# Kernel tuning notes

Measured on AMD Instinct MI355X. Metric: run time of the kernel, lower is better.

Reference implementation:

```python
import jax, jax.numpy as jnp
import numpy as np

B, S, D_IN = 256, 1024, 64
H, W_H = 256, 512
W_Y, D_OUT = 256, 64


def setup_inputs() -> dict:
    key = jax.random.key(0)
    ks = jax.random.split(key, 5)
    sc = lambda fan_in: 1.0 / np.sqrt(fan_in)
    return {
        "x": jax.random.normal(ks[0], (B, S, D_IN), dtype=jnp.float32),
        "W1h": jax.random.normal(ks[1], (H + D_IN, W_H), dtype=jnp.float32) * sc(H + D_IN),
        "b1h": jnp.zeros((W_H,), jnp.float32),
        "W2h": jax.random.normal(ks[2], (W_H, H), dtype=jnp.float32) * sc(W_H),
        "b2h": jnp.zeros((H,), jnp.float32),
        "W1y": jax.random.normal(ks[3], (H, W_Y), dtype=jnp.float32) * sc(H),
        "b1y": jnp.zeros((W_Y,), jnp.float32),
        "W2y": jax.random.normal(ks[4], (W_Y, D_OUT), dtype=jnp.float32) * sc(W_Y),
        "b2y": jnp.zeros((D_OUT,), jnp.float32),
    }


def reference(x, W1h, b1h, W2h, b2h, W1y, b1y, W2y, b2y):
    # h_t = hmlp([h_{t-1}, x_t]);  y_t = ymlp(h_t)
    batch = x.shape[0]
    h0 = jnp.zeros((batch, H), x.dtype)

    def step(h, x_t):
        hx = jnp.concatenate([h, x_t], axis=1)          # [B, H+D_IN]
        h_new = jax.nn.silu(hx @ W1h + b1h) @ W2h + b2h  # [B, H]
        y = jax.nn.silu(h_new @ W1y + b1y) @ W2y + b2y   # [B, D_OUT]
        return h_new, (y, h_new)

    xs = jnp.swapaxes(x, 0, 1)                          # [S, B, D_IN]
    _, (ys, hs) = jax.lax.scan(step, h0, xs)
    outs = jnp.swapaxes(ys, 0, 1)                        # [B, S, D_OUT]
    hiddens = jnp.concatenate([h0[None], hs], axis=0)    # [S+1, B, H]
    return outs, hiddens
```

## Files before the change

### kernel.cpp

```cpp
#include <hip/hip_runtime.h>


typedef __bf16 bf16;
typedef __bf16 bf16x8 __attribute__((ext_vector_type(8)));
typedef float  f32x4  __attribute__((ext_vector_type(4)));

#define MFMA16(a, b, c) __builtin_amdgcn_mfma_f32_16x16x32_bf16((a), (b), (c), 0, 0, 0)

static constexpr int Bz = 256, Sq = 1024, DIN = 64, H = 256, WH = 512, WY = 256, DOUT = 64;
static constexpr int OUTS_N = Bz * Sq * DOUT;
static constexpr int HID_T  = Bz * H;

static constexpr int W1H_OFF = 0;
static constexpr int W1H_CNT = (H + DIN) * WH;
static constexpr int W2H_OFF = W1H_OFF + W1H_CNT;
static constexpr int W2H_CNT = WH * H;
static constexpr int W1Y_OFF = W2H_OFF + W2H_CNT;
static constexpr int W1Y_CNT = H * WY;
static constexpr int W2Y_OFF = W1Y_OFF + W1Y_CNT;
static constexpr int W2Y_CNT = WY * DOUT;
static constexpr int PACK_TOTAL = W2Y_OFF + W2Y_CNT;

static constexpr int HX_LD = 328;
static constexpr int A1_LD = 520;
static constexpr int HB_LD = 264;

__device__ __forceinline__ float silu_f(float z) {
    return z / (1.0f + __expf(-z));
}

__global__ void prep_pack(const float* __restrict__ W1h, const float* __restrict__ W2h,
                          const float* __restrict__ W1y, const float* __restrict__ W2y,
                          bf16* __restrict__ ws) {
    int idx = blockIdx.x * 256 + threadIdx.x;
    if (idx >= PACK_TOTAL) return;
    int r = idx;
    const float* src; int row, col, ld;
    if (idx < W2H_OFF) {
        int j = r & 7; r >>= 3; int L = r & 63; r >>= 6;
        int kc = r % 10, nt = r / 10;
        row = kc * 32 + ((L >> 4) << 3) + j; col = nt * 16 + (L & 15);
        src = W1h; ld = WH;
    } else if (idx < W1Y_OFF) {
        r -= W2H_OFF;
        int j = r & 7; r >>= 3; int L = r & 63; r >>= 6;
        int kc = r & 15, nt = r >> 4;
        row = kc * 32 + ((L >> 4) << 3) + j; col = nt * 16 + (L & 15);
        src = W2h; ld = H;
    } else if (idx < W2Y_OFF) {
        r -= W1Y_OFF;
        int j = r & 7; r >>= 3; int L = r & 63; r >>= 6;
        int kc = r & 7, nt = r >> 3;
        row = kc * 32 + ((L >> 4) << 3) + j; col = nt * 16 + (L & 15);
        src = W1y; ld = WY;
    } else {
        r -= W2Y_OFF;
        int j = r & 7; r >>= 3; int L = r & 63; r >>= 6;
        int kc = r & 7, nt = r >> 3;
        row = kc * 32 + ((L >> 4) << 3) + j; col = nt * 16 + (L & 15);
        src = W2y; ld = DOUT;
    }
    ws[idx] = (bf16)src[row * ld + col];
}

__global__ __launch_bounds__(512, 2) void rnn_recur(
        const float* __restrict__ x, const float* __restrict__ b1h,
        const float* __restrict__ b2h, const bf16* __restrict__ ws,
        float* __restrict__ out) {
    __shared__ __align__(16) bf16 w2l[16 * 8 * 64 * 8];
    __shared__ __align__(16) bf16 hx_s[16 * HX_LD];
    __shared__ __align__(16) bf16 a1_s[16 * A1_LD];

    const int tid = threadIdx.x;
    const int wv = tid >> 6, ln = tid & 63;
    const int quad = ln >> 4, l16 = ln & 15;
    const int wgb = blockIdx.x;
    float* hid = out + OUTS_N;

    for (int i = tid; i < 16 * 256; i += 512) {
        int m = i >> 8, c = i & 255;
        hx_s[m * HX_LD + c] = (bf16)0.0f;
        hid[(wgb * 16 + m) * H + c] = 0.0f;
    }

    for (int u = tid; u < 16 * 8 * 64; u += 512) {
        int nt = u >> 9, kc8 = (u >> 6) & 7, lu = u & 63;
        *(bf16x8*)(w2l + ((size_t)u << 3)) =
            *(const bf16x8*)(ws + W2H_OFF + (((nt * 16 + 8 + kc8) * 64 + lu) << 3));
    }

    bf16x8 w1r[6][4];
#pragma unroll
    for (int kci = 0; kci < 6; kci++)
#pragma unroll
        for (int i = 0; i < 4; i++)
            w1r[kci][i] = *(const bf16x8*)(ws + W1H_OFF + ((((wv * 4 + i) * 10 + 4 + kci) * 64 + ln) << 3));

    bf16x8 w2f[8][2];
#pragma unroll
    for (int kc = 0; kc < 8; kc++)
#pragma unroll
        for (int i = 0; i < 2; i++)
            w2f[kc][i] = *(const bf16x8*)(ws + W2H_OFF + ((((wv * 2 + i) * 16 + kc) * 64 + ln) << 3));

    float bs1[4], bs2[2];
#pragma unroll
    for (int i = 0; i < 4; i++) bs1[i] = b1h[(wv * 4 + i) * 16 + l16];
#pragma unroll
    for (int i = 0; i < 2; i++) bs2[i] = b2h[(wv * 2 + i) * 16 + l16];

    const int mrow = tid >> 5;
    const int i2 = (tid & 31) * 2;
    const float* xrow = x + (size_t)(wgb * 16 + mrow) * (Sq * DIN) + i2;

#define W1HP(i, kc) ((const bf16x8*)(ws + W1H_OFF + ((((wv * 4 + (i)) * 10 + (kc)) * 64 + ln) << 3)))
    bf16x8 sA[4], sB[4];
#pragma unroll
    for (int i = 0; i < 4; i++) sA[i] = *W1HP(i, 0);
#pragma unroll
    for (int i = 0; i < 4; i++) sB[i] = *W1HP(i, 1);

    const f32x4 z4 = {0.0f, 0.0f, 0.0f, 0.0f};
    float2 xv = *(const float2*)(xrow);

#define LDHX(kc) (*(const bf16x8*)(hx_s + l16 * HX_LD + (kc) * 32 + quad * 8))
#define LDA1(kc) (*(const bf16x8*)(a1_s + l16 * A1_LD + (kc) * 32 + quad * 8))

#pragma unroll 1
    for (int t = 0; t < Sq; t++) {
        hx_s[mrow * HX_LD + 256 + i2]     = (bf16)xv.x;
        hx_s[mrow * HX_LD + 256 + i2 + 1] = (bf16)xv.y;
        __syncthreads();

        xv = *(const float2*)(xrow + ((t + 1) & (Sq - 1)) * DIN);

        f32x4 acc1[4] = {z4, z4, z4, z4};
        bf16x8 a;
        a = LDHX(0);
#pragma unroll
        for (int i = 0; i < 4; i++) acc1[i] = MFMA16(a, sA[i], acc1[i]);
#pragma unroll
        for (int i = 0; i < 4; i++) sA[i] = *W1HP(i, 2);
        a = LDHX(1);
#pragma unroll
        for (int i = 0; i < 4; i++) acc1[i] = MFMA16(a, sB[i], acc1[i]);
#pragma unroll
        for (int i = 0; i < 4; i++) sB[i] = *W1HP(i, 3);
        a = LDHX(4);
#pragma unroll
        for (int i = 0; i < 4; i++) acc1[i] = MFMA16(a, w1r[0][i], acc1[i]);
        a = LDHX(5);
#pragma unroll
        for (int i = 0; i < 4; i++) acc1[i] = MFMA16(a, w1r[1][i], acc1[i]);
        a = LDHX(2);
#pragma unroll
        for (int i = 0; i < 4; i++) acc1[i] = MFMA16(a, sA[i], acc1[i]);
        a = LDHX(3);
#pragma unroll
        for (int i = 0; i < 4; i++) acc1[i] = MFMA16(a, sB[i], acc1[i]);
        a = LDHX(6);
#pragma unroll
        for (int i = 0; i < 4; i++) acc1[i] = MFMA16(a, w1r[2][i], acc1[i]);
        a = LDHX(7);
#pragma unroll
        for (int i = 0; i < 4; i++) acc1[i] = MFMA16(a, w1r[3][i], acc1[i]);
        a = LDHX(8);
#pragma unroll
        for (int i = 0; i < 4; i++) acc1[i] = MFMA16(a, w1r[4][i], acc1[i]);
        a = LDHX(9);
#pragma unroll
        for (int i = 0; i < 4; i++) acc1[i] = MFMA16(a, w1r[5][i], acc1[i]);

#pragma unroll
        for (int i = 0; i < 4; i++)
#pragma unroll
            for (int r = 0; r < 4; r++) {
                float s = silu_f(acc1[i][r] + bs1[i]);
                a1_s[(quad * 4 + r) * A1_LD + (wv * 4 + i) * 16 + l16] = (bf16)s;
            }
        __syncthreads();

#pragma unroll
        for (int i = 0; i < 4; i++) sA[i] = *W1HP(i, 0);
#pragma unroll
        for (int i = 0; i < 4; i++) sB[i] = *W1HP(i, 1);

        f32x4 acc2[2] = {z4, z4};
#pragma unroll
        for (int kc = 0; kc < 8; kc++) {
            a = LDA1(kc);
#pragma unroll
            for (int i = 0; i < 2; i++) acc2[i] = MFMA16(a, w2f[kc][i], acc2[i]);
        }
#pragma unroll
        for (int kc = 8; kc < 16; kc++) {
            a = LDA1(kc);
#pragma unroll
            for (int i = 0; i < 2; i++) {
                bf16x8 b = *(const bf16x8*)(w2l + ((((wv * 2 + i) * 8 + (kc - 8)) * 64 + ln) << 3));
                acc2[i] = MFMA16(a, b, acc2[i]);
            }
        }

        float* hdst = hid + (size_t)(t + 1) * HID_T + (wgb * 16) * H;
#pragma unroll
        for (int i = 0; i < 2; i++)
#pragma unroll
            for (int r = 0; r < 4; r++) {
                float h = acc2[i][r] + bs2[i];
                int m = quad * 4 + r, c = (wv * 2 + i) * 16 + l16;
                hdst[m * H + c] = h;
                hx_s[m * HX_LD + c] = (bf16)h;
            }
    }
#undef W1HP
#undef LDHX
#undef LDA1
}

__global__ __launch_bounds__(256) void rnn_ymlp(
        const float* __restrict__ b1y, const float* __restrict__ b2y,
        const bf16* __restrict__ ws, float* __restrict__ out) {
    __shared__ __align__(16) bf16 hb[64 * HB_LD];

    const int tid = threadIdx.x, wv = tid >> 6, ln = tid & 63;
    const int quad = ln >> 4, l16 = ln & 15;
    const int g = blockIdx.x, b = g >> 4, t0 = (g & 15) * 64;
    const float* hid = out + OUTS_N;

    {
        int r = tid >> 2, c0 = (tid & 3) * 64;
        const float* srcr = hid + (size_t)(t0 + 1 + r) * HID_T + b * H + c0;
        bf16* d0 = hb + r * HB_LD + c0;
#pragma unroll
        for (int jj = 0; jj < 16; jj++) {
            float4 v = *(const float4*)(srcr + jj * 4);
            bf16* d = d0 + jj * 4;
            d[0] = (bf16)v.x; d[1] = (bf16)v.y; d[2] = (bf16)v.z; d[3] = (bf16)v.w;
        }
    }
    __syncthreads();

    const f32x4 z4 = {0.0f, 0.0f, 0.0f, 0.0f};
    f32x4 acc[4][4];
#pragma unroll
    for (int i = 0; i < 4; i++)
#pragma unroll
        for (int mt = 0; mt < 4; mt++) acc[i][mt] = z4;
#pragma unroll
    for (int kc = 0; kc < 8; kc++) {
        bf16x8 a[4];
#pragma unroll
        for (int mt = 0; mt < 4; mt++)
            a[mt] = *(const bf16x8*)(hb + (mt * 16 + l16) * HB_LD + kc * 32 + quad * 8);
#pragma unroll
        for (int i = 0; i < 4; i++) {
            bf16x8 bb = *(const bf16x8*)(ws + W1Y_OFF + ((((wv * 4 + i) * 8 + kc) * 64 + ln) << 3));
#pragma unroll
            for (int mt = 0; mt < 4; mt++) acc[i][mt] = MFMA16(a[mt], bb, acc[i][mt]);
        }
    }
    float bias1[4];
#pragma unroll
    for (int i = 0; i < 4; i++) bias1[i] = b1y[(wv * 4 + i) * 16 + l16];
    __syncthreads();

#pragma unroll
    for (int i = 0; i < 4; i++)
#pragma unroll
        for (int mt = 0; mt < 4; mt++)
#pragma unroll
            for (int r = 0; r < 4; r++) {
                float s = silu_f(acc[i][mt][r] + bias1[i]);
                hb[(mt * 16 + quad * 4 + r) * HB_LD + (wv * 4 + i) * 16 + l16] = (bf16)s;
            }
    __syncthreads();

    f32x4 acy[4] = {z4, z4, z4, z4};
#pragma unroll
    for (int kc = 0; kc < 8; kc++) {
        bf16x8 bb = *(const bf16x8*)(ws + W2Y_OFF + (((wv * 8 + kc) * 64 + ln) << 3));
#pragma unroll
        for (int mt = 0; mt < 4; mt++) {
            bf16x8 a = *(const bf16x8*)(hb + (mt * 16 + l16) * HB_LD + kc * 32 + quad * 8);
            acy[mt] = MFMA16(a, bb, acy[mt]);
        }
    }
    float bias2 = b2y[wv * 16 + l16];
    float* ob = out + (size_t)b * (Sq * DOUT);
#pragma unroll
    for (int mt = 0; mt < 4; mt++)
#pragma unroll
        for (int r = 0; r < 4; r++) {
            int m = mt * 16 + quad * 4 + r;
            ob[(t0 + m) * DOUT + wv * 16 + l16] = acy[mt][r] + bias2;
        }
}

extern "C" void kernel_launch(void* const* d_in, const int* in_sizes, int n_in,
                              void* d_out, int out_size, void* d_ws, size_t ws_size,
                              hipStream_t stream) {
    (void)in_sizes; (void)n_in; (void)out_size; (void)ws_size;
    const float* x   = (const float*)d_in[0];
    const float* W1h = (const float*)d_in[1];
    const float* b1h = (const float*)d_in[2];
    const float* W2h = (const float*)d_in[3];
    const float* b2h = (const float*)d_in[4];
    const float* W1y = (const float*)d_in[5];
    const float* b1y = (const float*)d_in[6];
    const float* W2y = (const float*)d_in[7];
    const float* b2y = (const float*)d_in[8];
    float* out = (float*)d_out;
    bf16* ws = (bf16*)d_ws;

    prep_pack<<<(PACK_TOTAL + 255) / 256, 256, 0, stream>>>(W1h, W2h, W1y, W2y, ws);
    rnn_recur<<<16, 512, 0, stream>>>(x, b1h, b2h, ws, out);
    rnn_ymlp<<<4096, 256, 0, stream>>>(b1y, b2y, ws, out);
}
```

Baseline: 4.449 ms.

## Transpose MFMA operands, XOR-swizzle LDS, vectorize stores, fold biases into accumulators

Swaps the A/B operands of every MFMA so each lane owns four consecutive output columns. That allows packed bf16x4 LDS writes and float4 global stores for hidden states and outputs in place of scalar stores. The padded LDS row strides are replaced by an XOR swizzle to avoid bank conflicts, and bias values now initialize the accumulators. One W1h chunk moves from registers to streamed loads, which frees registers but adds one more global load per step.

```diff
diff --git a/kernel.cpp b/kernel.cpp
--- a/kernel.cpp
+++ b/kernel.cpp
@@ -2,6 +2,8 @@
 
 
 typedef __bf16 bf16;
+typedef __bf16 bf16x2 __attribute__((ext_vector_type(2)));
+typedef __bf16 bf16x4 __attribute__((ext_vector_type(4)));
 typedef __bf16 bf16x8 __attribute__((ext_vector_type(8)));
 typedef float  f32x4  __attribute__((ext_vector_type(4)));
 
@@ -21,12 +23,17 @@
 static constexpr int W2Y_CNT = WY * DOUT;
 static constexpr int PACK_TOTAL = W2Y_OFF + W2Y_CNT;
 
-static constexpr int HX_LD = 328;
-static constexpr int A1_LD = 520;
-static constexpr int HB_LD = 264;
-
-__device__ __forceinline__ float silu_f(float z) {
-    return z / (1.0f + __expf(-z));
+static constexpr int HX_LD = 320;
+static constexpr int A1_LD = 512;
+
+__device__ __forceinline__ float silu_f(float z) { return z / (1.0f + __expf(-z)); }
+__device__ __forceinline__ int swz8(int row) { return ((row ^ (row >> 3)) & 7) << 3; }
+
+__device__ __forceinline__ bf16x4 silu4(f32x4 v) {
+    bf16x4 p;
+    p[0] = (bf16)silu_f(v[0]); p[1] = (bf16)silu_f(v[1]);
+    p[2] = (bf16)silu_f(v[2]); p[3] = (bf16)silu_f(v[3]);
+    return p;
 }
 
 __global__ void prep_pack(const float* __restrict__ W1h, const float* __restrict__ W2h,
@@ -74,12 +81,13 @@
     const int tid = threadIdx.x;
     const int wv = tid >> 6, ln = tid & 63;
     const int quad = ln >> 4, l16 = ln & 15;
+    const int swl = swz8(l16);
     const int wgb = blockIdx.x;
     float* hid = out + OUTS_N;
 
+    for (int i = tid; i < 16 * HX_LD; i += 512) hx_s[i] = (bf16)0.0f;
     for (int i = tid; i < 16 * 256; i += 512) {
         int m = i >> 8, c = i & 255;
-        hx_s[m * HX_LD + c] = (bf16)0.0f;
         hid[(wgb * 16 + m) * H + c] = 0.0f;
     }
 
@@ -89,12 +97,12 @@
             *(const bf16x8*)(ws + W2H_OFF + (((nt * 16 + 8 + kc8) * 64 + lu) << 3));
     }
 
-    bf16x8 w1r[6][4];
-#pragma unroll
-    for (int kci = 0; kci < 6; kci++)
+    bf16x8 w1r[5][4];
+#pragma unroll
+    for (int kci = 0; kci < 5; kci++)
 #pragma unroll
         for (int i = 0; i < 4; i++)
-            w1r[kci][i] = *(const bf16x8*)(ws + W1H_OFF + ((((wv * 4 + i) * 10 + 4 + kci) * 64 + ln) << 3));
+            w1r[kci][i] = *(const bf16x8*)(ws + W1H_OFF + ((((wv * 4 + i) * 10 + 5 + kci) * 64 + ln) << 3));
 
     bf16x8 w2f[8][2];
 #pragma unroll
@@ -103,15 +111,22 @@
         for (int i = 0; i < 2; i++)
             w2f[kc][i] = *(const bf16x8*)(ws + W2H_OFF + ((((wv * 2 + i) * 16 + kc) * 64 + ln) << 3));
 
-    float bs1[4], bs2[2];
-#pragma unroll
-    for (int i = 0; i < 4; i++) bs1[i] = b1h[(wv * 4 + i) * 16 + l16];
-#pragma unroll
-    for (int i = 0; i < 2; i++) bs2[i] = b2h[(wv * 2 + i) * 16 + l16];
+    f32x4 bs1[4], bs2[2];
+#pragma unroll
+    for (int i = 0; i < 4; i++) {
+        float4 v = *(const float4*)(b1h + (wv * 4 + i) * 16 + quad * 4);
+        bs1[i][0] = v.x; bs1[i][1] = v.y; bs1[i][2] = v.z; bs1[i][3] = v.w;
+    }
+#pragma unroll
+    for (int i = 0; i < 2; i++) {
+        float4 v = *(const float4*)(b2h + (wv * 2 + i) * 16 + quad * 4);
+        bs2[i][0] = v.x; bs2[i][1] = v.y; bs2[i][2] = v.z; bs2[i][3] = v.w;
+    }
 
     const int mrow = tid >> 5;
     const int i2 = (tid & 31) * 2;
     const float* xrow = x + (size_t)(wgb * 16 + mrow) * (Sq * DIN) + i2;
+    const int xoff = mrow * HX_LD + ((256 + i2) ^ swz8(mrow));
 
 #define W1HP(i, kc) ((const bf16x8*)(ws + W1H_OFF + ((((wv * 4 + (i)) * 10 + (kc)) * 64 + ln) << 3)))
     bf16x8 sA[4], sB[4];
@@ -120,64 +135,61 @@
 #pragma unroll
     for (int i = 0; i < 4; i++) sB[i] = *W1HP(i, 1);
 
-    const f32x4 z4 = {0.0f, 0.0f, 0.0f, 0.0f};
     float2 xv = *(const float2*)(xrow);
 
-#define LDHX(kc) (*(const bf16x8*)(hx_s + l16 * HX_LD + (kc) * 32 + quad * 8))
-#define LDA1(kc) (*(const bf16x8*)(a1_s + l16 * A1_LD + (kc) * 32 + quad * 8))
+#define LDHX(kc) (*(const bf16x8*)(hx_s + l16 * HX_LD + (((kc) * 32 + quad * 8) ^ swl)))
+#define LDA1(kc) (*(const bf16x8*)(a1_s + l16 * A1_LD + (((kc) * 32 + quad * 8) ^ swl)))
 
 #pragma unroll 1
     for (int t = 0; t < Sq; t++) {
-        hx_s[mrow * HX_LD + 256 + i2]     = (bf16)xv.x;
-        hx_s[mrow * HX_LD + 256 + i2 + 1] = (bf16)xv.y;
+        bf16x2 xp; xp[0] = (bf16)xv.x; xp[1] = (bf16)xv.y;
+        *(bf16x2*)(hx_s + xoff) = xp;
         __syncthreads();
 
         xv = *(const float2*)(xrow + ((t + 1) & (Sq - 1)) * DIN);
 
-        f32x4 acc1[4] = {z4, z4, z4, z4};
+        f32x4 acc1[4] = {bs1[0], bs1[1], bs1[2], bs1[3]};
         bf16x8 a;
         a = LDHX(0);
 #pragma unroll
-        for (int i = 0; i < 4; i++) acc1[i] = MFMA16(a, sA[i], acc1[i]);
+        for (int i = 0; i < 4; i++) acc1[i] = MFMA16(sA[i], a, acc1[i]);
 #pragma unroll
         for (int i = 0; i < 4; i++) sA[i] = *W1HP(i, 2);
         a = LDHX(1);
 #pragma unroll
-        for (int i = 0; i < 4; i++) acc1[i] = MFMA16(a, sB[i], acc1[i]);
+        for (int i = 0; i < 4; i++) acc1[i] = MFMA16(sB[i], a, acc1[i]);
 #pragma unroll
         for (int i = 0; i < 4; i++) sB[i] = *W1HP(i, 3);
+        a = LDHX(5);
+#pragma unroll
+        for (int i = 0; i < 4; i++) acc1[i] = MFMA16(w1r[0][i], a, acc1[i]);
+        a = LDHX(6);
+#pragma unroll
+        for (int i = 0; i < 4; i++) acc1[i] = MFMA16(w1r[1][i], a, acc1[i]);
+        a = LDHX(2);
+#pragma unroll
+        for (int i = 0; i < 4; i++) acc1[i] = MFMA16(sA[i], a, acc1[i]);
+#pragma unroll
+        for (int i = 0; i < 4; i++) sA[i] = *W1HP(i, 4);
+        a = LDHX(3);
+#pragma unroll
+        for (int i = 0; i < 4; i++) acc1[i] = MFMA16(sB[i], a, acc1[i]);
+        a = LDHX(7);
+#pragma unroll
+        for (int i = 0; i < 4; i++) acc1[i] = MFMA16(w1r[2][i], a, acc1[i]);
         a = LDHX(4);
 #pragma unroll
-        for (int i = 0; i < 4; i++) acc1[i] = MFMA16(a, w1r[0][i], acc1[i]);
-        a = LDHX(5);
-#pragma unroll
-        for (int i = 0; i < 4; i++) acc1[i] = MFMA16(a, w1r[1][i], acc1[i]);
-        a = LDHX(2);
-#pragma unroll
-        for (int i = 0; i < 4; i++) acc1[i] = MFMA16(a, sA[i], acc1[i]);
-        a = LDHX(3);
-#pragma unroll
-        for (int i = 0; i < 4; i++) acc1[i] = MFMA16(a, sB[i], acc1[i]);
-        a = LDHX(6);
-#pragma unroll
-        for (int i = 0; i < 4; i++) acc1[i] = MFMA16(a, w1r[2][i], acc1[i]);
-        a = LDHX(7);
-#pragma unroll
-        for (int i = 0; i < 4; i++) acc1[i] = MFMA16(a, w1r[3][i], acc1[i]);
+        for (int i = 0; i < 4; i++) acc1[i] = MFMA16(sA[i], a, acc1[i]);
         a = LDHX(8);
 #pragma unroll
-        for (int i = 0; i < 4; i++) acc1[i] = MFMA16(a, w1r[4][i], acc1[i]);
+        for (int i = 0; i < 4; i++) acc1[i] = MFMA16(w1r[3][i], a, acc1[i]);
         a = LDHX(9);
 #pragma unroll
-        for (int i = 0; i < 4; i++) acc1[i] = MFMA16(a, w1r[5][i], acc1[i]);
+        for (int i = 0; i < 4; i++) acc1[i] = MFMA16(w1r[4][i], a, acc1[i]);
 
 #pragma unroll
         for (int i = 0; i < 4; i++)
-#pragma unroll
-            for (int r = 0; r < 4; r++) {
-                float s = silu_f(acc1[i][r] + bs1[i]);
-                a1_s[(quad * 4 + r) * A1_LD + (wv * 4 + i) * 16 + l16] = (bf16)s;
-            }
+            *(bf16x4*)(a1_s + l16 * A1_LD + (((wv * 4 + i) * 16 + quad * 4) ^ swl)) = silu4(acc1[i]);
         __syncthreads();
 
 #pragma unroll
@@ -185,12 +197,12 @@
 #pragma unroll
         for (int i = 0; i < 4; i++) sB[i] = *W1HP(i, 1);
 
-        f32x4 acc2[2] = {z4, z4};
+        f32x4 acc2[2] = {bs2[0], bs2[1]};
 #pragma unroll
         for (int kc = 0; kc < 8; kc++) {
             a = LDA1(kc);
 #pragma unroll
-            for (int i = 0; i < 2; i++) acc2[i] = MFMA16(a, w2f[kc][i], acc2[i]);
+            for (int i = 0; i < 2; i++) acc2[i] = MFMA16(w2f[kc][i], a, acc2[i]);
         }
 #pragma unroll
         for (int kc = 8; kc < 16; kc++) {
@@ -198,20 +210,18 @@
 #pragma unroll
             for (int i = 0; i < 2; i++) {
                 bf16x8 b = *(const bf16x8*)(w2l + ((((wv * 2 + i) * 8 + (kc - 8)) * 64 + ln) << 3));
-                acc2[i] = MFMA16(a, b, acc2[i]);
+                acc2[i] = MFMA16(b, a, acc2[i]);
             }
         }
 
-        float* hdst = hid + (size_t)(t + 1) * HID_T + (wgb * 16) * H;
-#pragma unroll
-        for (int i = 0; i < 2; i++)
-#pragma unroll
-            for (int r = 0; r < 4; r++) {
-                float h = acc2[i][r] + bs2[i];
-                int m = quad * 4 + r, c = (wv * 2 + i) * 16 + l16;
-                hdst[m * H + c] = h;
-                hx_s[m * HX_LD + c] = (bf16)h;
-            }
+        float* hdst = hid + (size_t)(t + 1) * HID_T + (wgb * 16 + l16) * H;
+#pragma unroll
+        for (int i = 0; i < 2; i++) {
+            float4 hv; hv.x = acc2[i][0]; hv.y = acc2[i][1]; hv.z = acc2[i][2]; hv.w = acc2[i][3];
+            *(float4*)(hdst + (2 * wv + i) * 16 + quad * 4) = hv;
+            bf16x4 p; p[0] = (bf16)hv.x; p[1] = (bf16)hv.y; p[2] = (bf16)hv.z; p[3] = (bf16)hv.w;
+            *(bf16x4*)(hx_s + l16 * HX_LD + (((2 * wv + i) * 16 + quad * 4) ^ swl)) = p;
+        }
     }
 #undef W1HP
 #undef LDHX
@@ -221,7 +231,7 @@
 __global__ __launch_bounds__(256) void rnn_ymlp(
         const float* __restrict__ b1y, const float* __restrict__ b2y,
         const bf16* __restrict__ ws, float* __restrict__ out) {
-    __shared__ __align__(16) bf16 hb[64 * HB_LD];
+    __shared__ __align__(16) bf16 hb[64 * 256];
 
     const int tid = threadIdx.x, wv = tid >> 6, ln = tid & 63;
     const int quad = ln >> 4, l16 = ln & 15;
@@ -230,71 +240,75 @@
 
     {
         int r = tid >> 2, c0 = (tid & 3) * 64;
+        const int swr = swz8(r);
         const float* srcr = hid + (size_t)(t0 + 1 + r) * HID_T + b * H + c0;
-        bf16* d0 = hb + r * HB_LD + c0;
+        bf16* drow = hb + r * 256;
 #pragma unroll
         for (int jj = 0; jj < 16; jj++) {
             float4 v = *(const float4*)(srcr + jj * 4);
-            bf16* d = d0 + jj * 4;
-            d[0] = (bf16)v.x; d[1] = (bf16)v.y; d[2] = (bf16)v.z; d[3] = (bf16)v.w;
+            bf16x4 p; p[0] = (bf16)v.x; p[1] = (bf16)v.y; p[2] = (bf16)v.z; p[3] = (bf16)v.w;
+            *(bf16x4*)(drow + ((c0 + jj * 4) ^ swr)) = p;
         }
     }
     __syncthreads();
 
-    const f32x4 z4 = {0.0f, 0.0f, 0.0f, 0.0f};
     f32x4 acc[4][4];
 #pragma unroll
+    for (int i = 0; i < 4; i++) {
+        float4 v = *(const float4*)(b1y + (wv * 4 + i) * 16 + quad * 4);
+        f32x4 bv; bv[0] = v.x; bv[1] = v.y; bv[2] = v.z; bv[3] = v.w;
+#pragma unroll
+        for (int nt = 0; nt < 4; nt++) acc[i][nt] = bv;
+    }
+#pragma unroll
+    for (int kc = 0; kc < 8; kc++) {
+        bf16x8 bb[4];
+#pragma unroll
+        for (int nt = 0; nt < 4; nt++) {
+            int row = nt * 16 + l16;
+            bb[nt] = *(const bf16x8*)(hb + row * 256 + ((kc * 32 + quad * 8) ^ swz8(row)));
+        }
+#pragma unroll
+        for (int i = 0; i < 4; i++) {
+            bf16x8 wf = *(const bf16x8*)(ws + W1Y_OFF + ((((wv * 4 + i) * 8 + kc) * 64 + ln) << 3));
+#pragma unroll
+            for (int nt = 0; nt < 4; nt++) acc[i][nt] = MFMA16(wf, bb[nt], acc[i][nt]);
+        }
+    }
+    __syncthreads();
+
+#pragma unroll
     for (int i = 0; i < 4; i++)
 #pragma unroll
-        for (int mt = 0; mt < 4; mt++) acc[i][mt] = z4;
+        for (int nt = 0; nt < 4; nt++) {
+            int row = nt * 16 + l16;
+            *(bf16x4*)(hb + row * 256 + ((((wv * 4 + i) * 16 + quad * 4)) ^ swz8(row))) = silu4(acc[i][nt]);
+        }
+    __syncthreads();
+
+    f32x4 acy[4];
+    {
+        float4 v = *(const float4*)(b2y + wv * 16 + quad * 4);
+        f32x4 bv; bv[0] = v.x; bv[1] = v.y; bv[2] = v.z; bv[3] = v.w;
+#pragma unroll
+        for (int nt = 0; nt < 4; nt++) acy[nt] = bv;
+    }
 #pragma unroll
     for (int kc = 0; kc < 8; kc++) {
-        bf16x8 a[4];
-#pragma unroll
-        for (int mt = 0; mt < 4; mt++)
-            a[mt] = *(const bf16x8*)(hb + (mt * 16 + l16) * HB_LD + kc * 32 + quad * 8);
-#pragma unroll
-        for (int i = 0; i < 4; i++) {
-            bf16x8 bb = *(const bf16x8*)(ws + W1Y_OFF + ((((wv * 4 + i) * 8 + kc) * 64 + ln) << 3));
-#pragma unroll
-            for (int mt = 0; mt < 4; mt++) acc[i][mt] = MFMA16(a[mt], bb, acc[i][mt]);
-        }
-    }
-    float bias1[4];
-#pragma unroll
-    for (int i = 0; i < 4; i++) bias1[i] = b1y[(wv * 4 + i) * 16 + l16];
-    __syncthreads();
-
-#pragma unroll
-    for (int i = 0; i < 4; i++)
-#pragma unroll
-        for (int mt = 0; mt < 4; mt++)
-#pragma unroll
-            for (int r = 0; r < 4; r++) {
-                float s = silu_f(acc[i][mt][r] + bias1[i]);
-                hb[(mt * 16 + quad * 4 + r) * HB_LD + (wv * 4 + i) * 16 + l16] = (bf16)s;
-            }
-    __syncthreads();
-
-    f32x4 acy[4] = {z4, z4, z4, z4};
-#pragma unroll
-    for (int kc = 0; kc < 8; kc++) {
-        bf16x8 bb = *(const bf16x8*)(ws + W2Y_OFF + (((wv * 8 + kc) * 64 + ln) << 3));
-#pragma unroll
-        for (int mt = 0; mt < 4; mt++) {
-            bf16x8 a = *(const bf16x8*)(hb + (mt * 16 + l16) * HB_LD + kc * 32 + quad * 8);
-            acy[mt] = MFMA16(a, bb, acy[mt]);
-        }
-    }
-    float bias2 = b2y[wv * 16 + l16];
+        bf16x8 wf = *(const bf16x8*)(ws + W2Y_OFF + (((wv * 8 + kc) * 64 + ln) << 3));
+#pragma unroll
+        for (int nt = 0; nt < 4; nt++) {
+            int row = nt * 16 + l16;
+            bf16x8 aa = *(const bf16x8*)(hb + row * 256 + ((kc * 32 + quad * 8) ^ swz8(row)));
+            acy[nt] = MFMA16(wf, aa, acy[nt]);
+        }
+    }
     float* ob = out + (size_t)b * (Sq * DOUT);
 #pragma unroll
-    for (int mt = 0; mt < 4; mt++)
-#pragma unroll
-        for (int r = 0; r < 4; r++) {
-            int m = mt * 16 + quad * 4 + r;
-            ob[(t0 + m) * DOUT + wv * 16 + l16] = acy[mt][r] + bias2;
-        }
+    for (int nt = 0; nt < 4; nt++) {
+        float4 v; v.x = acy[nt][0]; v.y = acy[nt][1]; v.z = acy[nt][2]; v.w = acy[nt][3];
+        *(float4*)(ob + (size_t)(t0 + nt * 16 + l16) * DOUT + wv * 16 + quad * 4) = v;
+    }
 }
 
 extern "C" void kernel_launch(void* const* d_in, const int* in_sizes, int n_in,
```

Result: slower. 6.481 ms (+45.7%).
